# Kernel tuning notes

Measured on AMD Instinct MI355X. Metric: run time of the kernel, lower is better.

## Reference

```python
import jax, jax.numpy as jnp
import numpy as np

B, S, D, H, L = 8, 2048, 512, 8, 5
DK = D // H
SP = S - L + 1  # number of local windows


def setup_inputs() -> dict:
    key = jax.random.key(0)
    ks = jax.random.split(key, 5)
    scale = 1.0 / np.sqrt(D).astype(np.float32)
    return {
        "query": jax.random.normal(ks[0], (B, S, D), dtype=jnp.float32),
        "key": jax.random.normal(ks[1], (B, S, D), dtype=jnp.float32),
        "value": jax.random.normal(ks[2], (B, S, D), dtype=jnp.float32),
        "W0": jax.random.normal(ks[3], (D, D), dtype=jnp.float32) * scale,
        "b0": jnp.zeros((D,), dtype=jnp.float32),
        "Wout": jax.random.normal(ks[4], (D, D), dtype=jnp.float32) * scale,
        "bout": jnp.zeros((D,), dtype=jnp.float32),
    }


def _local_agg(x, weighted):
    # x: (B, S, D). Sliding-window aggregation over windows of length L.
    # scores[b, t, s] = <x[b, t+L-1], x[b, s]> / sqrt(D)  -- per the source:
    # matmul(x[:, L-1:], x^T) / sqrt(d_model)
    scores = jnp.einsum("btd,bsd->bts", x[:, L - 1:], x) / (float(D) ** 0.5)
    idx = jnp.arange(SP)[:, None] + jnp.arange(L)[None, :]  # (SP, L)
    # per-window softmax over the L local scores
    w = jax.nn.softmax(jnp.take_along_axis(scores, idx[None, :, :], axis=-1), axis=-1)  # (B, SP, L)
    win = x[:, idx]  # (B, SP, L, D) gathered windows
    if weighted:
        win = w[..., None] * win
    return jnp.sum(win, axis=2)  # (B, SP, D)


def reference(query, key, value, W0, b0, Wout, bout):
    # Bug-faithful: the source overwrites the weighted query with the raw
    # windows (`query = q_list`), so query windows are summed UNweighted;
    # key windows use the local softmax weights.
    q = _local_agg(query, weighted=False)  # (B, SP, D)
    k = _local_agg(key, weighted=True)     # (B, SP, D)
    v = value[:, L - 1:] @ W0 + b0         # linears[0], aligned to SP positions

    def heads(t):  # (B, SP, D) -> (B, H, SP, DK)
        return t.reshape(t.shape[0], t.shape[1], H, DK).transpose(0, 2, 1, 3)

    qh, kh, vh = heads(q), heads(k), heads(v)
    att = jax.nn.softmax(jnp.einsum("bhtd,bhsd->bhts", qh, kh) / (float(DK) ** 0.5), axis=-1)
    x = jnp.einsum("bhts,bhsd->bhtd", att, vh)  # (B, H, SP, DK)
    x = x.transpose(0, 2, 1, 3).reshape(q.shape[0], SP, D)
    return x @ Wout + bout  # linears[-1]
```

## Files before the change

### kernel.cpp

```cpp
#include <hip/hip_runtime.h>
#include <hip/hip_bf16.h>
#include <hip/hip_fp16.h>

#define B_ 8
#define S_ 2048
#define D_ 512
#define H_ 8
#define L_ 5
#define DK_ 64
#define SP_ 2044
#define SPAD_ 2048

typedef _Float16 f16_t;
typedef _Float16 f16x4 __attribute__((ext_vector_type(4)));
typedef _Float16 f16x8 __attribute__((ext_vector_type(8)));
typedef __fp16 fp16x2_b __attribute__((ext_vector_type(2)));
typedef float f32x4 __attribute__((ext_vector_type(4)));
typedef float f32x16 __attribute__((ext_vector_type(16)));
typedef unsigned int u32;

static __device__ __forceinline__ f32x4 mfma16(f16x8 a, f16x8 b, f32x4 c) {
    return __builtin_amdgcn_mfma_f32_16x16x32_f16(a, b, c, 0, 0, 0);
}
static __device__ __forceinline__ f32x16 mfma32(f16x8 a, f16x8 b, f32x16 c) {
    return __builtin_amdgcn_mfma_f32_32x32x16_f16(a, b, c, 0, 0, 0);
}

union U32H2 { u32 u; fp16x2_b h; };
union FRAG { uint4 u; f16x8 f; };

#define PIPE_FENCE() do {                              \
    __builtin_amdgcn_sched_barrier(0);                 \
    asm volatile("s_waitcnt lgkmcnt(0)");              \
    __builtin_amdgcn_sched_barrier(0);                 \
    __builtin_amdgcn_s_barrier();                      \
    __builtin_amdgcn_sched_barrier(0);                 \
} while (0)

static __device__ __forceinline__ void swap32(u32 a, u32 b, u32& r0, u32& r1, int hi) {
#if __has_builtin(__builtin_amdgcn_permlane32_swap)
    auto r = __builtin_amdgcn_permlane32_swap(a, b, false, false);
    r0 = r[0]; r1 = r[1];
#else
    u32 t = __shfl_xor(hi ? a : b, 32, 64);
    r0 = hi ? t : a;
    r1 = hi ? b : t;
#endif
}

__global__ __launch_bounds__(256) void k_convert_w(
    const float* __restrict__ W0, const float* __restrict__ Wout,
    f16_t* __restrict__ WT0, f16_t* __restrict__ WT1) {
    int idx = blockIdx.x * 256 + threadIdx.x;
    int which = idx >> 18;
    int e = idx & 0x3FFFF;
    int k = e >> 9, n = e & 511;
    const float* W = which ? Wout : W0;
    f16_t* WT = which ? WT1 : WT0;
    WT[n * 512 + k] = (f16_t)W[k * 512 + n];
}

__global__ __launch_bounds__(256) void k_prep(
    const float* __restrict__ Qin, const float* __restrict__ Kin,
    f16_t* __restrict__ qh, f16_t* __restrict__ kh) {
    const int lane = threadIdx.x & 63;
    const int wid = threadIdx.x >> 6;
    const int gw = blockIdx.x * 4 + wid;
    const int b = gw >> 11;
    const int t = gw & 2047;
    const float* qb = Qin + (size_t)b * S_ * D_;
    const float* kb = Kin + (size_t)b * S_ * D_;
    const int d0 = lane * 8;

    float qs[8];
    float kl[5][8];
#pragma unroll
    for (int e = 0; e < 8; e++) qs[e] = 0.f;
#pragma unroll
    for (int l = 0; l < L_; l++) {
        int row = t + l; row = row < 2047 ? row : 2047;
        const float4* qp = (const float4*)(qb + (size_t)row * D_ + d0);
        float4 a = qp[0], c = qp[1];
        qs[0] += a.x; qs[1] += a.y; qs[2] += a.z; qs[3] += a.w;
        qs[4] += c.x; qs[5] += c.y; qs[6] += c.z; qs[7] += c.w;
        const float4* kp = (const float4*)(kb + (size_t)row * D_ + d0);
        float4 ka = kp[0], kc = kp[1];
        kl[l][0] = ka.x; kl[l][1] = ka.y; kl[l][2] = ka.z; kl[l][3] = ka.w;
        kl[l][4] = kc.x; kl[l][5] = kc.y; kl[l][6] = kc.z; kl[l][7] = kc.w;
    }
    float dot[5];
#pragma unroll
    for (int l = 0; l < 5; l++) {
        float d = 0.f;
#pragma unroll
        for (int e = 0; e < 8; e++) d += kl[4][e] * kl[l][e];
        dot[l] = d;
    }
#pragma unroll
    for (int m = 32; m; m >>= 1) {
#pragma unroll
        for (int l = 0; l < 5; l++) dot[l] += __shfl_xor(dot[l], m, 64);
    }
    const float sc = 0.044194173824159216f;
    float mx = dot[0];
#pragma unroll
    for (int l = 1; l < 5; l++) mx = fmaxf(mx, dot[l]);
    float w[5], sum = 0.f;
#pragma unroll
    for (int l = 0; l < 5; l++) { w[l] = __expf((dot[l] - mx) * sc); sum += w[l]; }
    float inv = 1.f / sum;
    float ks[8];
#pragma unroll
    for (int e = 0; e < 8; e++) {
        float v = 0.f;
#pragma unroll
        for (int l = 0; l < 5; l++) v += w[l] * kl[l][e];
        ks[e] = v * inv;
    }
    const int h = d0 >> 6, dk = d0 & 63;
    const size_t ob = ((size_t)(b * H_ + h) * SPAD_ + t) * DK_ + dk;
    const float qscale = 0.125f * 1.4426950408889634f;
    f16x8 qpk, kpk;
#pragma unroll
    for (int e = 0; e < 8; e++) {
        qpk[e] = (f16_t)(qs[e] * qscale);
        kpk[e] = (f16_t)ks[e];
    }
    *(f16x8*)(qh + ob) = qpk;
    *(f16x8*)(kh + ob) = kpk;
}

template <int MODE>
__global__ __launch_bounds__(256) void k_gemm(
    const void* __restrict__ Aptr, const f16_t* __restrict__ WT,
    const float* __restrict__ bias, void* __restrict__ Cptr) {
    __shared__ alignas(16) char smem[40960];
    const int tid = threadIdx.x, lane = tid & 63, wid = tid >> 6;
    const int mt = blockIdx.x >> 2, nt = blockIdx.x & 3;
    const int m0 = mt * 128, n0 = nt * 128;
    const int l15 = lane & 15, lg = lane >> 4;
    f32x4 acc[2][8] = {};

    const float* a0src = nullptr;
    const f16_t* a1src0 = nullptr, *a1src1 = nullptr;
    if (MODE == 0) {
        const float* A = (const float*)Aptr;
        int r = tid >> 1, cb = (tid & 1) * 16;
        int rp = m0 + r, b = rp >> 11, t = rp & 2047;
        int vrow = t + 4; vrow = vrow < 2047 ? vrow : 2047;
        a0src = A + ((size_t)b * 2048 + vrow) * 512 + cb;
    } else {
        const f16_t* A = (const f16_t*)Aptr;
        int r0 = tid >> 2, off0 = (tid & 3) * 8;
        int r1 = (tid + 256) >> 2;
        a1src0 = A + (size_t)(m0 + r0) * 512 + off0;
        a1src1 = A + (size_t)(m0 + r1) * 512 + off0;
    }
    const int bnl0 = tid >> 2, bko0 = (tid & 3) * 8;
    const int bnl1 = (tid + 256) >> 2;
    const f16_t* bsrc0 = WT + (size_t)(n0 + bnl0) * 512 + bko0;
    const f16_t* bsrc1 = WT + (size_t)(n0 + bnl1) * 512 + bko0;

    float4 fa[4];
    uint4 ua0, ua1, ub0, ub1;
    if (MODE == 0) {
#pragma unroll
        for (int j = 0; j < 4; j++) fa[j] = *(const float4*)(a0src + j * 4);
    } else {
        ua0 = *(const uint4*)a1src0;
        ua1 = *(const uint4*)a1src1;
    }
    ub0 = *(const uint4*)bsrc0;
    ub1 = *(const uint4*)bsrc1;

    auto stage = [&](int buf) {
        f16_t (*Asm)[40] = (f16_t(*)[40])(smem + buf * 10240);
        f16_t (*Bsm)[40] = (f16_t(*)[40])(smem + 20480 + buf * 10240);
        if (MODE == 0) {
            int r = tid >> 1, cb = (tid & 1) * 16;
            f16x8 p0, p1;
            p0[0] = (f16_t)fa[0].x; p0[1] = (f16_t)fa[0].y; p0[2] = (f16_t)fa[0].z; p0[3] = (f16_t)fa[0].w;
            p0[4] = (f16_t)fa[1].x; p0[5] = (f16_t)fa[1].y; p0[6] = (f16_t)fa[1].z; p0[7] = (f16_t)fa[1].w;
            p1[0] = (f16_t)fa[2].x; p1[1] = (f16_t)fa[2].y; p1[2] = (f16_t)fa[2].z; p1[3] = (f16_t)fa[2].w;
            p1[4] = (f16_t)fa[3].x; p1[5] = (f16_t)fa[3].y; p1[6] = (f16_t)fa[3].z; p1[7] = (f16_t)fa[3].w;
            *(f16x8*)&Asm[r][cb] = p0;
            *(f16x8*)&Asm[r][cb + 8] = p1;
        } else {
            int r0 = tid >> 2, r1 = (tid + 256) >> 2, off = (tid & 3) * 8;
            *(uint4*)&Asm[r0][off] = ua0;
            *(uint4*)&Asm[r1][off] = ua1;
        }
        *(uint4*)&Bsm[bnl0][bko0] = ub0;
        *(uint4*)&Bsm[bnl1][bko0] = ub1;
    };
    auto fetch = [&](int kt) {
        const int k0n = kt * 32;
        if (MODE == 0) {
#pragma unroll
            for (int j = 0; j < 4; j++) fa[j] = *(const float4*)(a0src + k0n + j * 4);
        } else {
            ua0 = *(const uint4*)(a1src0 + k0n);
            ua1 = *(const uint4*)(a1src1 + k0n);
        }
        ub0 = *(const uint4*)(bsrc0 + k0n);
        ub1 = *(const uint4*)(bsrc1 + k0n);
    };

    stage(0);
    fetch(1);
    PIPE_FENCE();

    for (int kt = 0; kt < 16; ++kt) {
        const int cur = kt & 1;
        f16_t (*Asm)[40] = (f16_t(*)[40])(smem + cur * 10240);
        f16_t (*Bsm)[40] = (f16_t(*)[40])(smem + 20480 + cur * 10240);
        f16x8 af[2], bfr[8];
#pragma unroll
        for (int i = 0; i < 2; i++) af[i] = *(const f16x8*)&Asm[wid * 32 + i * 16 + l15][lg * 8];
#pragma unroll
        for (int c = 0; c < 8; c++) bfr[c] = *(const f16x8*)&Bsm[c * 16 + l15][lg * 8];
        __builtin_amdgcn_s_setprio(1);
#pragma unroll
        for (int i = 0; i < 2; i++) {
#pragma unroll
            for (int c = 0; c < 8; c++) acc[i][c] = mfma16(af[i], bfr[c], acc[i][c]);
        }
        __builtin_amdgcn_s_setprio(0);
        if (kt < 15) {
            stage(cur ^ 1);
            if (kt < 14) fetch(kt + 2);
            PIPE_FENCE();
        }
    }

    if (MODE == 0) {
        __syncthreads();
        f16_t (*Csm)[136] = (f16_t(*)[136])smem;
#pragma unroll
        for (int i = 0; i < 2; i++) {
#pragma unroll
            for (int c = 0; c < 8; c++) {
                int col = n0 + c * 16 + l15;
                float bv = bias[col];
                f16x4 pk;
#pragma unroll
                for (int r = 0; r < 4; r++) pk[r] = (f16_t)(acc[i][c][r] + bv);
                *(f16x4*)&Csm[c * 16 + l15][wid * 32 + i * 16 + lg * 4] = pk;
            }
        }
        __syncthreads();
        const int b = m0 >> 11, t0 = m0 & 2047;
        const int cl = tid >> 1, mo = (tid & 1) * 64;
        const int h = (n0 + cl) >> 6, dk = (n0 + cl) & 63;
        f16_t* dst = (f16_t*)Cptr + ((size_t)(b * H_ + h) * DK_ + dk) * SPAD_ + t0 + mo;
#pragma unroll
        for (int j = 0; j < 8; j++)
            *(uint4*)(dst + j * 8) = *(const uint4*)&Csm[cl][mo + j * 8];
    } else {
#pragma unroll
        for (int i = 0; i < 2; i++) {
#pragma unroll
            for (int c = 0; c < 8; c++) {
#pragma unroll
                for (int r = 0; r < 4; r++) {
                    int row = m0 + wid * 32 + i * 16 + lg * 4 + r;
                    int col = n0 + c * 16 + l15;
                    float v = acc[i][c][r] + bias[col];
                    int b = row >> 11, t = row & 2047;
                    if (t < SP_) {
                        float* outp = (float*)Cptr;
                        outp[((size_t)b * SP_ + t) * 512 + col] = v;
                    }
                }
            }
        }
    }
}

__global__ __launch_bounds__(256, 4) void k_attn(
    const f16_t* __restrict__ qh, const f16_t* __restrict__ kh,
    const f16_t* __restrict__ vhT, f16_t* __restrict__ xatt) {
    __shared__ alignas(16) f16_t Ksm[2][64][68];
    __shared__ alignas(16) f16_t Vsm[2][64][68];
    const int tid = threadIdx.x, lane = tid & 63, wid = tid >> 6;
    const int l31 = lane & 31, hi = lane >> 5, hi8 = hi * 8;
    const int vb = ((blockIdx.x & 7) << 7) | (blockIdx.x >> 3);
    const int bh = vb >> 4, qt = vb & 15;
    const f16_t* Q = qh + (size_t)bh * SPAD_ * DK_;
    const f16_t* K = kh + (size_t)bh * SPAD_ * DK_;
    const f16_t* VT = vhT + (size_t)bh * DK_ * SPAD_;
    const int qw = qt * 128 + wid * 32;

    f16x8 qf[4];
#pragma unroll
    for (int kf = 0; kf < 4; kf++)
        qf[kf] = *(const f16x8*)(Q + (size_t)(qw + l31) * DK_ + kf * 16 + hi8);

    f32x16 cinit;
#pragma unroll
    for (int i = 0; i < 16; i++) cinit[i] = -12.f;

    f32x16 acc[2] = {};
    float rsa = 0.f, rsb = 0.f;
    u32 pk[2][8];
    U32H2 one2; one2.u = 0x3C003C00u;

    const int sr = tid >> 3, so = (tid & 7) * 8;
    const f16_t* kg0 = K + (size_t)sr * DK_ + so;
    const f16_t* kg1 = K + (size_t)(sr + 32) * DK_ + so;
    const f16_t* vg0 = VT + (size_t)sr * SPAD_ + so;
    const f16_t* vg1 = VT + (size_t)(sr + 32) * SPAD_ + so;

    uint4 rk0 = *(const uint4*)kg0;
    uint4 rk1 = *(const uint4*)kg1;
    uint4 rv0 = *(const uint4*)vg0;
    uint4 rv1 = *(const uint4*)vg1;
    *(uint4*)&Ksm[0][sr][so]      = rk0;
    *(uint4*)&Ksm[0][sr + 32][so] = rk1;
    *(uint4*)&Vsm[0][sr][so]      = rv0;
    *(uint4*)&Vsm[0][sr + 32][so] = rv1;
    rk0 = *(const uint4*)(kg0 + (size_t)64 * DK_);
    rk1 = *(const uint4*)(kg1 + (size_t)64 * DK_);
    rv0 = *(const uint4*)(vg0 + 64);
    rv1 = *(const uint4*)(vg1 + 64);
    PIPE_FENCE();

    for (int t = 0; t < 32; ++t) {
        const int cur = t & 1;

#pragma unroll
        for (int kr = 0; kr < 2; ++kr) {
            f32x16 sv = cinit;
            __builtin_amdgcn_s_setprio(1);
#pragma unroll
            for (int kf = 0; kf < 4; ++kf) {
                f16x8 a = *(const f16x8*)&Ksm[cur][kr * 32 + l31][kf * 16 + hi8];
                sv = mfma32(a, qf[kf], sv);
            }
            __builtin_amdgcn_s_setprio(0);
            if (t == 31 && kr == 1) {
#pragma unroll
                for (int r = 12; r < 16; ++r) sv[r] = hi ? -1e30f : sv[r];
            }
#pragma unroll
            for (int j = 0; j < 8; ++j) {
                float a0 = __builtin_amdgcn_exp2f(sv[2 * j]);
                float a1 = __builtin_amdgcn_exp2f(sv[2 * j + 1]);
                U32H2 c0; c0.h = __builtin_amdgcn_cvt_pkrtz(a0, a1);
                pk[kr][j] = c0.u;
#if __has_builtin(__builtin_amdgcn_fdot2)
                if (j & 1) rsb = __builtin_amdgcn_fdot2(c0.h, one2.h, rsb, false);
                else       rsa = __builtin_amdgcn_fdot2(c0.h, one2.h, rsa, false);
#else
                if (j & 1) rsb += a0 + a1;
                else       rsa += a0 + a1;
#endif
            }
        }

#pragma unroll
        for (int kc = 0; kc < 4; ++kc) {
            const int kr = kc >> 1, al = (kc & 1) * 4;
            FRAG p;
            {
                u32 m0, m1, m2, m3;
                swap32(pk[kr][al],     pk[kr][al + 2], m0, m2, hi);
                swap32(pk[kr][al + 1], pk[kr][al + 3], m1, m3, hi);
                p.u = make_uint4(m0, m1, m2, m3);
            }
            __builtin_amdgcn_s_setprio(1);
#pragma unroll
            for (int dc = 0; dc < 2; ++dc) {
                f16x8 v = *(const f16x8*)&Vsm[cur][dc * 32 + l31][kc * 16 + hi8];
                acc[dc] = mfma32(v, p.f, acc[dc]);
            }
            __builtin_amdgcn_s_setprio(0);
        }

        if (t < 31) {
            const int nb = cur ^ 1;
            *(uint4*)&Ksm[nb][sr][so]      = rk0;
            *(uint4*)&Ksm[nb][sr + 32][so] = rk1;
            *(uint4*)&Vsm[nb][sr][so]      = rv0;
            *(uint4*)&Vsm[nb][sr + 32][so] = rv1;
            if (t < 30) {
                const int nxt = (t + 2) << 6;
                rk0 = *(const uint4*)(kg0 + (size_t)nxt * DK_);
                rk1 = *(const uint4*)(kg1 + (size_t)nxt * DK_);
                rv0 = *(const uint4*)(vg0 + nxt);
                rv1 = *(const uint4*)(vg1 + nxt);
            }
            PIPE_FENCE();
        }
    }

    float rs = rsa + rsb;
    rs += __shfl_xor(rs, 32, 64);
    const float inv = 1.f / rs;

    __syncthreads();
    f16_t (*Osm)[68] = (f16_t(*)[68])&Ksm[0][0][0];
    {
        const int row = wid * 32 + l31;
#pragma unroll
        for (int dc = 0; dc < 2; ++dc) {
#pragma unroll
            for (int p = 0; p < 8; ++p) {
                float e0 = acc[dc][2 * p] * inv;
                float e1 = acc[dc][2 * p + 1] * inv;
                U32H2 c; c.h = __builtin_amdgcn_cvt_pkrtz(e0, e1);
                const int d = dc * 32 + 2 * (p & 1) + 8 * (p >> 1) + 4 * hi;
                *(u32*)&Osm[row][d] = c.u;
            }
        }
    }
    __syncthreads();
    const int b = bh >> 3, hh = bh & 7;
#pragma unroll
    for (int j = 0; j < 4; ++j) {
        const int lin = tid + j * 256;
        const int row = lin >> 3, dco = (lin & 7) * 8;
        uint4 v = *(const uint4*)&Osm[row][dco];
        f16_t* dst = xatt + ((size_t)b * SPAD_ + qt * 128 + row) * D_ + hh * DK_ + dco;
        *(uint4*)dst = v;
    }
}

extern "C" void kernel_launch(void* const* d_in, const int* in_sizes, int n_in,
                              void* d_out, int out_size, void* d_ws, size_t ws_size,
                              hipStream_t stream) {
    const float* query = (const float*)d_in[0];
    const float* key   = (const float*)d_in[1];
    const float* value = (const float*)d_in[2];
    const float* W0    = (const float*)d_in[3];
    const float* b0    = (const float*)d_in[4];
    const float* Wout  = (const float*)d_in[5];
    const float* bout  = (const float*)d_in[6];
    float* out = (float*)d_out;

    char* w = (char*)d_ws;
    const size_t SZ = (size_t)B_ * H_ * SPAD_ * DK_ * sizeof(f16_t);
    f16_t* qh   = (f16_t*)w; w += SZ;
    f16_t* kh   = (f16_t*)w; w += SZ;
    f16_t* vhT  = (f16_t*)w; w += SZ;
    f16_t* xatt = (f16_t*)w; w += SZ;
    f16_t* WT0  = (f16_t*)w; w += (size_t)512 * 512 * sizeof(f16_t);
    f16_t* WT1  = (f16_t*)w; w += (size_t)512 * 512 * sizeof(f16_t);

    k_convert_w<<<2048, 256, 0, stream>>>(W0, Wout, WT0, WT1);
    k_prep<<<4096, 256, 0, stream>>>(query, key, qh, kh);
    k_gemm<0><<<512, 256, 0, stream>>>((const void*)value, WT0, b0, (void*)vhT);
    k_attn<<<1024, 256, 0, stream>>>(qh, kh, vhT, xatt);
    k_gemm<1><<<512, 256, 0, stream>>>((const void*)xatt, WT1, bout, (void*)out);
}
```

Baseline: 160.5 us.

## Software-pipeline attention so QK of one tile overlaps PV of the previous

The attention loop is restructured so each iteration runs the QK MFMAs for tile t, then the PV MFMAs for tile t-1, then the exponentials. Staging of K and V is split and offset by one tile, with a separate prologue and epilogue. The goal is to hide exp/convert VALU work and LDS latency behind matrix instructions. The projection GEMM loop is also rewritten to stage the current buffer and prefetch the next k-slice with one __syncthreads per step. This raises register pressure and shortens the load lead time in the GEMM.

```diff
diff --git a/kernel.cpp b/kernel.cpp
--- a/kernel.cpp
+++ b/kernel.cpp
@@ -29,10 +29,9 @@
 union U32H2 { u32 u; fp16x2_b h; };
 union FRAG { uint4 u; f16x8 f; };
 
-#define PIPE_FENCE() do {                              \
+#define LGKMBAR() do {                                 \
     __builtin_amdgcn_sched_barrier(0);                 \
     asm volatile("s_waitcnt lgkmcnt(0)");              \
-    __builtin_amdgcn_sched_barrier(0);                 \
     __builtin_amdgcn_s_barrier();                      \
     __builtin_amdgcn_sched_barrier(0);                 \
 } while (0)
@@ -173,9 +172,10 @@
     ub0 = *(const uint4*)bsrc0;
     ub1 = *(const uint4*)bsrc1;
 
-    auto stage = [&](int buf) {
-        f16_t (*Asm)[40] = (f16_t(*)[40])(smem + buf * 10240);
-        f16_t (*Bsm)[40] = (f16_t(*)[40])(smem + 20480 + buf * 10240);
+    for (int kt = 0; kt < 16; ++kt) {
+        const int cur = kt & 1;
+        f16_t (*Asm)[40] = (f16_t(*)[40])(smem + cur * 10240);
+        f16_t (*Bsm)[40] = (f16_t(*)[40])(smem + 20480 + cur * 10240);
         if (MODE == 0) {
             int r = tid >> 1, cb = (tid & 1) * 16;
             f16x8 p0, p1;
@@ -192,28 +192,19 @@
         }
         *(uint4*)&Bsm[bnl0][bko0] = ub0;
         *(uint4*)&Bsm[bnl1][bko0] = ub1;
-    };
-    auto fetch = [&](int kt) {
-        const int k0n = kt * 32;
-        if (MODE == 0) {
-#pragma unroll
-            for (int j = 0; j < 4; j++) fa[j] = *(const float4*)(a0src + k0n + j * 4);
-        } else {
-            ua0 = *(const uint4*)(a1src0 + k0n);
-            ua1 = *(const uint4*)(a1src1 + k0n);
-        }
-        ub0 = *(const uint4*)(bsrc0 + k0n);
-        ub1 = *(const uint4*)(bsrc1 + k0n);
-    };
-
-    stage(0);
-    fetch(1);
-    PIPE_FENCE();
-
-    for (int kt = 0; kt < 16; ++kt) {
-        const int cur = kt & 1;
-        f16_t (*Asm)[40] = (f16_t(*)[40])(smem + cur * 10240);
-        f16_t (*Bsm)[40] = (f16_t(*)[40])(smem + 20480 + cur * 10240);
+        if (kt < 15) {
+            const int k0n = (kt + 1) * 32;
+            if (MODE == 0) {
+#pragma unroll
+                for (int j = 0; j < 4; j++) fa[j] = *(const float4*)(a0src + k0n + j * 4);
+            } else {
+                ua0 = *(const uint4*)(a1src0 + k0n);
+                ua1 = *(const uint4*)(a1src1 + k0n);
+            }
+            ub0 = *(const uint4*)(bsrc0 + k0n);
+            ub1 = *(const uint4*)(bsrc1 + k0n);
+        }
+        __syncthreads();
         f16x8 af[2], bfr[8];
 #pragma unroll
         for (int i = 0; i < 2; i++) af[i] = *(const f16x8*)&Asm[wid * 32 + i * 16 + l15][lg * 8];
@@ -226,11 +217,6 @@
             for (int c = 0; c < 8; c++) acc[i][c] = mfma16(af[i], bfr[c], acc[i][c]);
         }
         __builtin_amdgcn_s_setprio(0);
-        if (kt < 15) {
-            stage(cur ^ 1);
-            if (kt < 14) fetch(kt + 2);
-            PIPE_FENCE();
-        }
     }
 
     if (MODE == 0) {
@@ -291,18 +277,19 @@
     const f16_t* VT = vhT + (size_t)bh * DK_ * SPAD_;
     const int qw = qt * 128 + wid * 32;
 
-    f16x8 qf[4];
-#pragma unroll
-    for (int kf = 0; kf < 4; kf++)
-        qf[kf] = *(const f16x8*)(Q + (size_t)(qw + l31) * DK_ + kf * 16 + hi8);
+    f16x8 qf0 = *(const f16x8*)(Q + (size_t)(qw + l31) * DK_ + 0  + hi8);
+    f16x8 qf1 = *(const f16x8*)(Q + (size_t)(qw + l31) * DK_ + 16 + hi8);
+    f16x8 qf2 = *(const f16x8*)(Q + (size_t)(qw + l31) * DK_ + 32 + hi8);
+    f16x8 qf3 = *(const f16x8*)(Q + (size_t)(qw + l31) * DK_ + 48 + hi8);
 
     f32x16 cinit;
 #pragma unroll
     for (int i = 0; i < 16; i++) cinit[i] = -12.f;
 
-    f32x16 acc[2] = {};
+    f32x16 accA = {}, accB = {};
+    f32x16 sv;
     float rsa = 0.f, rsb = 0.f;
-    u32 pk[2][8];
+    uint4 pk0, pk1, pk2, pk3;
     U32H2 one2; one2.u = 0x3C003C00u;
 
     const int sr = tid >> 3, so = (tid & 7) * 8;
@@ -310,89 +297,125 @@
     const f16_t* kg1 = K + (size_t)(sr + 32) * DK_ + so;
     const f16_t* vg0 = VT + (size_t)sr * SPAD_ + so;
     const f16_t* vg1 = VT + (size_t)(sr + 32) * SPAD_ + so;
-
-    uint4 rk0 = *(const uint4*)kg0;
-    uint4 rk1 = *(const uint4*)kg1;
-    uint4 rv0 = *(const uint4*)vg0;
-    uint4 rv1 = *(const uint4*)vg1;
-    *(uint4*)&Ksm[0][sr][so]      = rk0;
-    *(uint4*)&Ksm[0][sr + 32][so] = rk1;
-    *(uint4*)&Vsm[0][sr][so]      = rv0;
-    *(uint4*)&Vsm[0][sr + 32][so] = rv1;
-    rk0 = *(const uint4*)(kg0 + (size_t)64 * DK_);
-    rk1 = *(const uint4*)(kg1 + (size_t)64 * DK_);
-    rv0 = *(const uint4*)(vg0 + 64);
-    rv1 = *(const uint4*)(vg1 + 64);
-    PIPE_FENCE();
-
-    for (int t = 0; t < 32; ++t) {
+    uint4 rk0, rk1, rv0, rv1;
+
+#define FETCH_K(T) do { const int o_ = (T) << 6;                          \
+    rk0 = *(const uint4*)(kg0 + (size_t)o_ * DK_);                        \
+    rk1 = *(const uint4*)(kg1 + (size_t)o_ * DK_); } while (0)
+#define FETCH_V(T) do { const int o_ = (T) << 6;                          \
+    rv0 = *(const uint4*)(vg0 + o_);                                      \
+    rv1 = *(const uint4*)(vg1 + o_); } while (0)
+#define STAGE_K(BUF) do {                                                 \
+    *(uint4*)&Ksm[BUF][sr][so] = rk0;                                     \
+    *(uint4*)&Ksm[BUF][sr + 32][so] = rk1; } while (0)
+#define STAGE_V(BUF) do {                                                 \
+    *(uint4*)&Vsm[BUF][sr][so] = rv0;                                     \
+    *(uint4*)&Vsm[BUF][sr + 32][so] = rv1; } while (0)
+
+#define QK_HALF(KB, ROW) do {                                             \
+    sv = cinit;                                                           \
+    __builtin_amdgcn_s_setprio(1);                                        \
+    {                                                                     \
+        f16x8 a0_ = *(const f16x8*)&Ksm[KB][(ROW)][0  + hi8];             \
+        sv = mfma32(a0_, qf0, sv);                                        \
+        f16x8 a1_ = *(const f16x8*)&Ksm[KB][(ROW)][16 + hi8];             \
+        sv = mfma32(a1_, qf1, sv);                                        \
+        f16x8 a2_ = *(const f16x8*)&Ksm[KB][(ROW)][32 + hi8];             \
+        sv = mfma32(a2_, qf2, sv);                                        \
+        f16x8 a3_ = *(const f16x8*)&Ksm[KB][(ROW)][48 + hi8];             \
+        sv = mfma32(a3_, qf3, sv);                                        \
+    }                                                                     \
+    __builtin_amdgcn_s_setprio(0);                                        \
+} while (0)
+
+#if __has_builtin(__builtin_amdgcn_fdot2)
+#define EXPPAIR(J, T, RS) do {                                            \
+    float e0_ = __builtin_amdgcn_exp2f(sv[2 * (J)]);                      \
+    float e1_ = __builtin_amdgcn_exp2f(sv[2 * (J) + 1]);                  \
+    U32H2 c_; c_.h = __builtin_amdgcn_cvt_pkrtz(e0_, e1_);                \
+    T = c_.u;                                                             \
+    RS = __builtin_amdgcn_fdot2(c_.h, one2.h, RS, false);                 \
+} while (0)
+#else
+#define EXPPAIR(J, T, RS) do {                                            \
+    float e0_ = __builtin_amdgcn_exp2f(sv[2 * (J)]);                      \
+    float e1_ = __builtin_amdgcn_exp2f(sv[2 * (J) + 1]);                  \
+    U32H2 c_; c_.h = __builtin_amdgcn_cvt_pkrtz(e0_, e1_);                \
+    T = c_.u;                                                             \
+    RS += e0_ + e1_;                                                      \
+} while (0)
+#endif
+
+#define EXP_HALF(PLO, PHI) do {                                           \
+    u32 t0_, t1_, t2_, t3_, t4_, t5_, t6_, t7_;                           \
+    EXPPAIR(0, t0_, rsa); EXPPAIR(1, t1_, rsb);                           \
+    EXPPAIR(2, t2_, rsa); EXPPAIR(3, t3_, rsb);                           \
+    EXPPAIR(4, t4_, rsa); EXPPAIR(5, t5_, rsb);                           \
+    EXPPAIR(6, t6_, rsa); EXPPAIR(7, t7_, rsb);                           \
+    PLO = make_uint4(t0_, t1_, t2_, t3_);                                 \
+    PHI = make_uint4(t4_, t5_, t6_, t7_);                                 \
+} while (0)
+
+#define PV_KC(VB, PKU, KC) do {                                           \
+    u32 m0_, m1_, m2_, m3_;                                               \
+    swap32(PKU.x, PKU.z, m0_, m2_, hi);                                   \
+    swap32(PKU.y, PKU.w, m1_, m3_, hi);                                   \
+    FRAG p_; p_.u = make_uint4(m0_, m1_, m2_, m3_);                       \
+    __builtin_amdgcn_s_setprio(1);                                        \
+    {                                                                     \
+        f16x8 v0_ = *(const f16x8*)&Vsm[VB][l31][(KC) * 16 + hi8];        \
+        accA = mfma32(v0_, p_.f, accA);                                   \
+        f16x8 v1_ = *(const f16x8*)&Vsm[VB][32 + l31][(KC) * 16 + hi8];   \
+        accB = mfma32(v1_, p_.f, accB);                                   \
+    }                                                                     \
+    __builtin_amdgcn_s_setprio(0);                                        \
+} while (0)
+
+#define PV_TILE(VB) do {                                                  \
+    PV_KC(VB, pk0, 0); PV_KC(VB, pk1, 1);                                 \
+    PV_KC(VB, pk2, 2); PV_KC(VB, pk3, 3);                                 \
+} while (0)
+
+    FETCH_K(0);
+    STAGE_K(0);
+    FETCH_K(1);
+    FETCH_V(0);
+    LGKMBAR();
+
+    QK_HALF(0, l31);
+    EXP_HALF(pk0, pk1);
+    QK_HALF(0, 32 + l31);
+    EXP_HALF(pk2, pk3);
+    STAGE_K(1);
+    STAGE_V(0);
+    FETCH_K(2);
+    FETCH_V(1);
+    LGKMBAR();
+
+    for (int t = 1; t <= 30; ++t) {
         const int cur = t & 1;
-
-#pragma unroll
-        for (int kr = 0; kr < 2; ++kr) {
-            f32x16 sv = cinit;
-            __builtin_amdgcn_s_setprio(1);
-#pragma unroll
-            for (int kf = 0; kf < 4; ++kf) {
-                f16x8 a = *(const f16x8*)&Ksm[cur][kr * 32 + l31][kf * 16 + hi8];
-                sv = mfma32(a, qf[kf], sv);
-            }
-            __builtin_amdgcn_s_setprio(0);
-            if (t == 31 && kr == 1) {
-#pragma unroll
-                for (int r = 12; r < 16; ++r) sv[r] = hi ? -1e30f : sv[r];
-            }
-#pragma unroll
-            for (int j = 0; j < 8; ++j) {
-                float a0 = __builtin_amdgcn_exp2f(sv[2 * j]);
-                float a1 = __builtin_amdgcn_exp2f(sv[2 * j + 1]);
-                U32H2 c0; c0.h = __builtin_amdgcn_cvt_pkrtz(a0, a1);
-                pk[kr][j] = c0.u;
-#if __has_builtin(__builtin_amdgcn_fdot2)
-                if (j & 1) rsb = __builtin_amdgcn_fdot2(c0.h, one2.h, rsb, false);
-                else       rsa = __builtin_amdgcn_fdot2(c0.h, one2.h, rsa, false);
-#else
-                if (j & 1) rsb += a0 + a1;
-                else       rsa += a0 + a1;
-#endif
-            }
-        }
-
-#pragma unroll
-        for (int kc = 0; kc < 4; ++kc) {
-            const int kr = kc >> 1, al = (kc & 1) * 4;
-            FRAG p;
-            {
-                u32 m0, m1, m2, m3;
-                swap32(pk[kr][al],     pk[kr][al + 2], m0, m2, hi);
-                swap32(pk[kr][al + 1], pk[kr][al + 3], m1, m3, hi);
-                p.u = make_uint4(m0, m1, m2, m3);
-            }
-            __builtin_amdgcn_s_setprio(1);
-#pragma unroll
-            for (int dc = 0; dc < 2; ++dc) {
-                f16x8 v = *(const f16x8*)&Vsm[cur][dc * 32 + l31][kc * 16 + hi8];
-                acc[dc] = mfma32(v, p.f, acc[dc]);
-            }
-            __builtin_amdgcn_s_setprio(0);
-        }
-
-        if (t < 31) {
-            const int nb = cur ^ 1;
-            *(uint4*)&Ksm[nb][sr][so]      = rk0;
-            *(uint4*)&Ksm[nb][sr + 32][so] = rk1;
-            *(uint4*)&Vsm[nb][sr][so]      = rv0;
-            *(uint4*)&Vsm[nb][sr + 32][so] = rv1;
-            if (t < 30) {
-                const int nxt = (t + 2) << 6;
-                rk0 = *(const uint4*)(kg0 + (size_t)nxt * DK_);
-                rk1 = *(const uint4*)(kg1 + (size_t)nxt * DK_);
-                rv0 = *(const uint4*)(vg0 + nxt);
-                rv1 = *(const uint4*)(vg1 + nxt);
-            }
-            PIPE_FENCE();
-        }
-    }
+        QK_HALF(cur, l31);
+        PV_TILE(cur ^ 1);
+        EXP_HALF(pk0, pk1);
+        QK_HALF(cur, 32 + l31);
+        EXP_HALF(pk2, pk3);
+        STAGE_K(cur ^ 1);
+        STAGE_V(cur);
+        if (t < 30) FETCH_K(t + 2);
+        FETCH_V(t + 1);
+        LGKMBAR();
+    }
+
+    QK_HALF(1, l31);
+    PV_TILE(0);
+    EXP_HALF(pk0, pk1);
+    QK_HALF(1, 32 + l31);
+#pragma unroll
+    for (int r = 12; r < 16; ++r) sv[r] = hi ? -1e30f : sv[r];
+    EXP_HALF(pk2, pk3);
+    STAGE_V(1);
+    LGKMBAR();
+    PV_TILE(1);
 
     float rs = rsa + rsb;
     rs += __shfl_xor(rs, 32, 64);
@@ -403,15 +426,20 @@
     {
         const int row = wid * 32 + l31;
 #pragma unroll
-        for (int dc = 0; dc < 2; ++dc) {
-#pragma unroll
-            for (int p = 0; p < 8; ++p) {
-                float e0 = acc[dc][2 * p] * inv;
-                float e1 = acc[dc][2 * p + 1] * inv;
-                U32H2 c; c.h = __builtin_amdgcn_cvt_pkrtz(e0, e1);
-                const int d = dc * 32 + 2 * (p & 1) + 8 * (p >> 1) + 4 * hi;
-                *(u32*)&Osm[row][d] = c.u;
-            }
+        for (int p = 0; p < 8; ++p) {
+            float e0 = accA[2 * p] * inv;
+            float e1 = accA[2 * p + 1] * inv;
+            U32H2 c; c.h = __builtin_amdgcn_cvt_pkrtz(e0, e1);
+            const int d = 2 * (p & 1) + 8 * (p >> 1) + 4 * hi;
+            *(u32*)&Osm[row][d] = c.u;
+        }
+#pragma unroll
+        for (int p = 0; p < 8; ++p) {
+            float e0 = accB[2 * p] * inv;
+            float e1 = accB[2 * p + 1] * inv;
+            U32H2 c; c.h = __builtin_amdgcn_cvt_pkrtz(e0, e1);
+            const int d = 32 + 2 * (p & 1) + 8 * (p >> 1) + 4 * hi;
+            *(u32*)&Osm[row][d] = c.u;
         }
     }
     __syncthreads();
@@ -424,6 +452,15 @@
         f16_t* dst = xatt + ((size_t)b * SPAD_ + qt * 128 + row) * D_ + hh * DK_ + dco;
         *(uint4*)dst = v;
     }
+#undef FETCH_K
+#undef FETCH_V
+#undef STAGE_K
+#undef STAGE_V
+#undef QK_HALF
+#undef EXPPAIR
+#undef EXP_HALF
+#undef PV_KC
+#undef PV_TILE
 }
 
 extern "C" void kernel_launch(void* const* d_in, const int* in_sizes, int n_in,
```

After: 526.1 us. 3.28x slower.
